# Optimization experiments

Measured on AMD Instinct MI355X. Metric: run time of the kernel, lower is better.

The kernel has to match this reference:

```python
import jax, jax.numpy as jnp
import numpy as np

EPS = 1e-5
K = 3  # involution kernel size


def bin_act(x):
    # STE binary activation: forward = sign(x), backward via piecewise poly
    m1 = (x < -1).astype(jnp.float32)
    m2 = (x < 0).astype(jnp.float32)
    m3 = (x < 1).astype(jnp.float32)
    out = -1.0 * m1 + (x * x + 2 * x) * (1 - m1)
    out = out * m2 + (-x * x + 2 * x) * (1 - m2)
    out = out * m3 + 1.0 * (1 - m3)
    sg = jax.lax.stop_gradient
    return sg(jnp.sign(x)) - sg(out) + out


def bin_conv1x1(x, w):
    # BinaryConv with kernel_size=1: w is (O, I, 1, 1)
    sf = jnp.mean(jnp.abs(w), axis=(1, 2, 3), keepdims=True)
    bw = sf * jnp.sign(w)
    rw = jnp.clip(w, -1.0, 1.0)
    sg = jax.lax.stop_gradient
    f = sg(bw) - sg(rw) + rw  # (O, I, 1, 1)
    return jnp.einsum('oi,bihw->bohw', f[:, :, 0, 0], x)


def batchnorm(x, gamma, beta):
    # training-mode BN over (N, H, W) per channel, biased variance
    m = jnp.mean(x, axis=(0, 2, 3), keepdims=True)
    v = jnp.mean((x - m) ** 2, axis=(0, 2, 3), keepdims=True)
    xn = (x - m) * jax.lax.rsqrt(v + EPS)
    return gamma.reshape(1, -1, 1, 1) * xn + beta.reshape(1, -1, 1, 1)


def prelu(x, a):
    return jnp.maximum(x, 0) + a.reshape(1, -1, 1, 1) * jnp.minimum(x, 0)


def setup_inputs() -> dict:
    key = jax.random.key(0)
    ks = jax.random.split(key, 8)
    B, C, H, W = 8, 64, 128, 128
    Cr = C // 2           # reduce_rate = 2
    KK = K * K            # group = 1
    inp = {
        'x': jax.random.normal(ks[0], (B, C, H, W), dtype=jnp.float32),
        'pre_bias_b': jnp.zeros((1, C, 1, 1), jnp.float32),
        'pre_conv_w': jax.random.uniform(ks[1], (C, C, 1, 1), jnp.float32) * 0.001,
        'pre_gamma': jnp.ones((C,), jnp.float32),
        'pre_beta': jnp.zeros((C,), jnp.float32),
        'pre_a': jnp.full((C,), 0.25, jnp.float32),
        'mid_bias_b': jnp.zeros((1, C, 1, 1), jnp.float32),
        'reduce_w': jax.random.uniform(ks[2], (Cr, C, 1, 1), jnp.float32) * 0.001,
        'span_w': jax.random.uniform(ks[3], (KK, Cr, 1, 1), jnp.float32) * 0.001,
        'mid_gamma': jnp.ones((C,), jnp.float32),
        'mid_beta': jnp.zeros((C,), jnp.float32),
        'mid_a': jnp.full((C,), 0.25, jnp.float32),
        'post_bias_b': jnp.zeros((1, C, 1, 1), jnp.float32),
        'post_conv_w': jax.random.uniform(ks[4], (C, C, 1, 1), jnp.float32) * 0.001,
        'post_gamma': jnp.ones((C,), jnp.float32),
        'post_beta': jnp.zeros((C,), jnp.float32),
    }
    return inp


def reference(x, pre_bias_b, pre_conv_w, pre_gamma, pre_beta, pre_a,
              mid_bias_b, reduce_w, span_w, mid_gamma, mid_beta, mid_a,
              post_bias_b, post_conv_w, post_gamma, post_beta):
    B, C, H, W = x.shape
    h = bin_act(x)
    h = h + pre_bias_b
    h = bin_conv1x1(h, pre_conv_w)
    h = batchnorm(h, pre_gamma, pre_beta)
    h = prelu(h, pre_a)
    h = h + mid_bias_b
    # kernel branch (AvgPool2d(1,1) is identity for stride=1)
    ker = bin_conv1x1(bin_conv1x1(h, reduce_w), span_w)  # (B, K*K, H, W)
    # unfold: 3x3 patches, pad=1, stride=1 -> (B, C, K*K, H, W)
    hp = jnp.pad(h, ((0, 0), (0, 0), (1, 1), (1, 1)))
    patches = jnp.stack(
        [hp[:, :, i:i + H, j:j + W] for i in range(K) for j in range(K)],
        axis=2)
    out = jnp.sum(patches * ker[:, None, :, :, :], axis=2)  # (B, C, H, W)
    out = batchnorm(out, mid_gamma, mid_beta)
    out = jax.nn.relu(out)
    out = prelu(out, mid_a)
    out = out + post_bias_b
    out = bin_conv1x1(out, post_conv_w)
    out = batchnorm(out, post_gamma, post_beta)
    return out + x  # downsample is Identity (stride=1)
```

## Files before the change

### kernel.cpp

```cpp
#include <hip/hip_runtime.h>

#define B_   8
#define HW   16384
#define CHW  (64*HW)
#define NPIX (8*16384)
#define EPS_ 1e-5f

typedef unsigned short u16;
typedef unsigned int   u32;
typedef unsigned long long u64;
typedef __attribute__((ext_vector_type(8))) short bf16x8;
typedef __attribute__((ext_vector_type(4))) float f32x4;

__device__ __forceinline__ float sgnf(float v){ return (float)((v>0.f)-(v<0.f)); }
__device__ __forceinline__ float bf2f(u16 h){ return __uint_as_float(((u32)h)<<16); }
__device__ __forceinline__ u16 f2bf(float f){
    u32 u = __float_as_uint(f);
    u += 0x7fffu + ((u>>16)&1u);
    return (u16)(u>>16);
}
__device__ __forceinline__ u32 pack2(float a, float b){
    return (u32)f2bf(a) | ((u32)f2bf(b)<<16);
}

__device__ __forceinline__ void bn1_consts(const u32* __restrict__ cnt,
                                           const float* __restrict__ AB,
                                           const float* __restrict__ g,
                                           const float* __restrict__ be,
                                           const float* __restrict__ pa,
                                           const float* __restrict__ mb,
                                           float* kA, float* kB,
                                           float* al, float* mbl, int tid){
    if (tid < 64){
        float A  = AB[tid], Bv = AB[64+tid];
        float sp = (float)cnt[tid], sq = (float)cnt[64+tid];
        float mpc = sp * (1.f/(float)NPIX);
        float e2  = sq * (1.f/(float)NPIX);
        float mean = fmaf(A, mpc, Bv);
        float var  = A*A*fmaxf(e2 - mpc*mpc, 0.f);
        float sc = g[tid] * rsqrtf(var + EPS_);
        float sh = be[tid] - mean*sc;
        kA[tid] = sc*A;
        kB[tid] = fmaf(sc, Bv, sh);
        al[tid] = pa[tid];
        mbl[tid]= mb[tid];
    }
}

__global__ __launch_bounds__(576) void prep(
                     const float* __restrict__ pre_w, const float* __restrict__ pre_bias,
                     const float* __restrict__ red_w, const float* __restrict__ span_w,
                     const float* __restrict__ post_w,
                     u32* __restrict__ wb, float* __restrict__ AB,
                     u16* __restrict__ wqbf, float* __restrict__ M,
                     u32* __restrict__ cnt){
    __shared__ float sr[32], ss[9];
    int t = threadIdx.x;
    if (t < 128) cnt[t] = 0u;
    if (t < 64){
        float s = 0.f;
        for (int i = 0; i < 64; i++) s += fabsf(pre_w[t*64+i]);
        float alpha = s * (1.f/64.f);
        u32 b0 = 0, b1 = 0;
        for (int i = 0; i < 32; i++){
            b0 |= (__float_as_uint(pre_w[t*64+i])    >> 31) << i;
            b1 |= (__float_as_uint(pre_w[t*64+32+i]) >> 31) << i;
        }
        float c0 = 0.f;
        for (int i = 0; i < 64; i++)
            c0 += alpha * sgnf(pre_w[t*64+i]) * pre_bias[i];
        wb[2*t]   = b0;
        wb[2*t+1] = b1;
        AB[t]     = -2.f * alpha;
        AB[64+t]  = 64.f * alpha + c0;
    }
    if (t >= 64 && t < 128){
        int o = t - 64;
        float s2 = 0.f;
        for (int i = 0; i < 64; i++) s2 += fabsf(post_w[o*64+i]);
        s2 *= (1.f/64.f);
        for (int i = 0; i < 64; i++) wqbf[o*64+i] = f2bf(s2 * sgnf(post_w[o*64+i]));
    }
    if (t >= 128 && t < 160){
        int r = t - 128;
        float s = 0.f;
        for (int i = 0; i < 64; i++) s += fabsf(red_w[r*64+i]);
        sr[r] = s * (1.f/64.f);
    }
    if (t >= 160 && t < 169){
        int j = t - 160;
        float s = 0.f;
        for (int r = 0; r < 32; r++) s += fabsf(span_w[j*32+r]);
        ss[j] = s * (1.f/32.f);
    }
    __syncthreads();
    if (t < 576){
        int i = t / 9, j = t - (t/9)*9;
        float m = 0.f;
        for (int r = 0; r < 32; r++)
            m += sgnf(span_w[j*32+r]) * sr[r] * sgnf(red_w[r*64+i]);
        M[i*9+j] = ss[j] * m;
    }
}

__global__ __launch_bounds__(256) void packb(const float* __restrict__ x,
                                             const u32* __restrict__ wb,
                                             u32* __restrict__ cnt,
                                             uint2* __restrict__ sb){
    __shared__ u32 blo[4][64], bhi[4][64];
    __shared__ uint2 sbl[256];
    __shared__ u32 ps[256], qs[256];
    int tid  = threadIdx.x;
    int w    = tid >> 6, lane = tid & 63;
    int p0   = blockIdx.x*256 + w*64;
    int b    = p0 >> 14;
    int pix  = p0 & (HW-1);
    const float* xb = x + (size_t)b*CHW + pix + lane;

    float v[64];
#pragma unroll
    for (int c = 0; c < 64; c++) v[c] = xb[(size_t)c*HW];

#pragma unroll
    for (int c = 0; c < 64; c++){
        u64 bal = __ballot((int)(__float_as_uint(v[c]) >> 31));
        if (lane == c){
            blo[w][c] = (u32)bal;
            bhi[w][c] = (u32)(bal >> 32);
        }
    }
    __syncthreads();

    u32 m0 = 0, m1 = 0;
    int sh = lane & 31;
    bool hi = lane >= 32;
#pragma unroll
    for (int c = 0; c < 32; c++){
        u32 sel = hi ? bhi[w][c] : blo[w][c];
        m0 |= ((sel >> sh) & 1u) << c;
    }
#pragma unroll
    for (int c = 0; c < 32; c++){
        u32 sel = hi ? bhi[w][32+c] : blo[w][32+c];
        m1 |= ((sel >> sh) & 1u) << c;
    }
    sb[p0 + lane] = make_uint2(m0, m1);
    sbl[tid]      = make_uint2(m0, m1);
    __syncthreads();

    int o  = tid & 63;
    int qd = tid >> 6;
    u32 w0 = wb[2*o], w1 = wb[2*o+1];
    u32 sp = 0, sq = 0;
#pragma unroll 8
    for (int k = 0; k < 64; k++){
        uint2 vv = sbl[qd*64 + k];
        u32 pc = (u32)(__popc(vv.x ^ w0) + __popc(vv.y ^ w1));
        sp += pc;
        sq += pc*pc;
    }
    ps[qd*64 + o] = sp;
    qs[qd*64 + o] = sq;
    __syncthreads();
    if (tid < 64){
        u32 S = ps[tid] + ps[64+tid] + ps[128+tid] + ps[192+tid];
        u32 Q = qs[tid] + qs[64+tid] + qs[128+tid] + qs[192+tid];
        atomicAdd(&cnt[tid],    S);
        atomicAdd(&cnt[64+tid], Q);
    }
}

__global__ __launch_bounds__(256) void kerk(const uint2* __restrict__ sb,
                                            const u32* __restrict__ cnt,
                                            const float* __restrict__ AB,
                                            const u32* __restrict__ wb,
                                            const float* __restrict__ pre_g,
                                            const float* __restrict__ pre_b,
                                            const float* __restrict__ pa,
                                            const float* __restrict__ mb,
                                            const float* __restrict__ M,
                                            u16* __restrict__ ker){
    __shared__ float kA[64], kB[64], al[64], mbl[64];
    __shared__ u32 wbl[128];
    int tid = threadIdx.x;
    bn1_consts(cnt, AB, pre_g, pre_b, pa, mb, kA, kB, al, mbl, tid);
    if (tid < 128) wbl[tid] = wb[tid];
    __syncthreads();

    int p   = blockIdx.x*256 + tid;
    int b   = p >> 14;
    int pix = p & (HW-1);
    uint2 mv = sb[p];

    float acc[9];
#pragma unroll
    for (int j = 0; j < 9; j++) acc[j] = 0.f;
    for (int i = 0; i < 64; i++){
        u32 pc = (u32)(__popc(mv.x ^ wbl[2*i]) + __popc(mv.y ^ wbl[2*i+1]));
        float w = fmaf(kA[i], (float)pc, kB[i]);
        float z = fmaxf(w, 0.f) + al[i]*fminf(w, 0.f) + mbl[i];
#pragma unroll
        for (int j = 0; j < 9; j++)
            acc[j] = fmaf(M[i*9+j], z, acc[j]);
    }
    u16* kb = ker + (size_t)b*9*HW + pix;
#pragma unroll
    for (int j = 0; j < 9; j++) kb[(size_t)j*HW] = f2bf(acc[j]);
}

__global__ __launch_bounds__(256) void gatherk(const uint2* __restrict__ sb,
                                               const u32* __restrict__ cnt,
                                               const float* __restrict__ AB,
                                               const u32* __restrict__ wb,
                                               const float* __restrict__ pre_g,
                                               const float* __restrict__ pre_b,
                                               const float* __restrict__ pa,
                                               const float* __restrict__ mb,
                                               const u16* __restrict__ ker,
                                               u16* __restrict__ y2,
                                               float2* __restrict__ part2){
    __shared__ float kA[64], kB[64], al[64], mbl[64];
    __shared__ u32 wbl[128];
    __shared__ uint2 sbT[768];
    __shared__ float zr[8*6*132];
    __shared__ float2 rowsum[32];

    int tid = threadIdx.x;
    bn1_consts(cnt, AB, pre_g, pre_b, pa, mb, kA, kB, al, mbl, tid);
    if (tid < 128) wbl[tid] = wb[tid];
    if (tid < 96){
        int cc = tid / 12, rem = tid - cc*12, rr = rem >> 1, ed = rem & 1;
        zr[(cc*6 + rr)*132 + ed*129] = 0.f;
    }

    int bid = blockIdx.x;
    int b  = bid >> 8;
    int cg = (bid >> 5) & 7;
    int rg = bid & 31;
    int y0 = rg*4;
    int c0 = cg*8;

    const uint2* sbb = sb + (size_t)b*HW;
#pragma unroll
    for (int k = 0; k < 3; k++){
        int e  = tid + 256*k;
        int rr = e >> 7;
        int xx = e & 127;
        int gy = y0 + rr - 1;
        int gc = min(max(gy, 0), 127);
        sbT[e] = sbb[gc*128 + xx];
    }
    __syncthreads();

#pragma unroll
    for (int k = 0; k < 24; k++){
        int e  = tid + 256*k;
        int cc = e / 768;
        int r2 = e - cc*768;
        int rr = r2 >> 7;
        int xx = r2 & 127;
        int c  = c0 + cc;
        int gy = y0 + rr - 1;
        float z = 0.f;
        if ((unsigned)gy < 128u){
            uint2 v = sbT[rr*128 + xx];
            u32 pc = (u32)(__popc(v.x ^ wbl[2*c]) + __popc(v.y ^ wbl[2*c+1]));
            float w = fmaf(kA[c], (float)pc, kB[c]);
            z = fmaxf(w, 0.f) + al[c]*fminf(w, 0.f) + mbl[c];
        }
        zr[(cc*6 + rr)*132 + xx + 1] = z;
    }
    __syncthreads();

    {
        int lane2 = tid & 63;
        int wv    = tid >> 6;
        int x0    = lane2*2;
        int gp    = (y0 + wv)*128 + x0;

        float k0[9], k1[9];
        const u16* kb = ker + (size_t)b*9*HW + gp;
#pragma unroll
        for (int j = 0; j < 9; j++){
            u32 u = *reinterpret_cast<const u32*>(kb + (size_t)j*HW);
            k0[j] = __uint_as_float(u << 16);
            k1[j] = __uint_as_float(u & 0xffff0000u);
        }

        u32* yo = reinterpret_cast<u32*>(y2 + (size_t)(b*64 + c0)*HW + gp);
#pragma unroll
        for (int cc = 0; cc < 8; cc++){
            const float* zrow = &zr[(cc*6 + wv)*132 + x0];
            float o0 = 0.f, o1 = 0.f;
#pragma unroll
            for (int dy = 0; dy < 3; dy++){
                float2 za = *reinterpret_cast<const float2*>(zrow + dy*132);
                float2 zb = *reinterpret_cast<const float2*>(zrow + dy*132 + 2);
                o0 = fmaf(za.x, k0[dy*3+0], o0);
                o0 = fmaf(za.y, k0[dy*3+1], o0);
                o0 = fmaf(zb.x, k0[dy*3+2], o0);
                o1 = fmaf(za.y, k1[dy*3+0], o1);
                o1 = fmaf(zb.x, k1[dy*3+1], o1);
                o1 = fmaf(zb.y, k1[dy*3+2], o1);
            }
            yo[(size_t)cc*(HW/2)] = pack2(o0, o1);
            float sm = o0 + o1, qm = o0*o0 + o1*o1;
#pragma unroll
            for (int m = 1; m < 64; m <<= 1){
                sm += __shfl_xor(sm, m);
                qm += __shfl_xor(qm, m);
            }
            if (lane2 == 0) rowsum[wv*8 + cc] = make_float2(sm, qm);
        }
    }
    __syncthreads();
    if (tid < 8){
        float S = 0.f, Q = 0.f;
#pragma unroll
        for (int w = 0; w < 4; w++){
            float2 v = rowsum[w*8 + tid];
            S += v.x; Q += v.y;
        }
        part2[(size_t)(c0 + tid)*256 + (b*32 + rg)] = make_float2(S, Q);
    }
}

__global__ __launch_bounds__(256) void combinek(const float2* __restrict__ part,
                                                const float* __restrict__ gamma,
                                                const float* __restrict__ beta,
                                                float* __restrict__ scsh,
                                                int nsl){
    int c = blockIdx.x, tid = threadIdx.x;
    float S = 0.f, Q = 0.f;
    for (int k = tid; k < nsl; k += 256){
        float2 v = part[(size_t)c*nsl + k];
        S += v.x; Q += v.y;
    }
    for (int off = 32; off > 0; off >>= 1){
        S += __shfl_down(S, off);
        Q += __shfl_down(Q, off);
    }
    __shared__ float2 wp[4];
    if ((tid & 63) == 0) wp[tid>>6] = make_float2(S, Q);
    __syncthreads();
    if (tid == 0){
        float S2 = 0.f, Q2 = 0.f;
#pragma unroll
        for (int w = 0; w < 4; w++){ S2 += wp[w].x; Q2 += wp[w].y; }
        float mean = S2 * (1.f/(float)NPIX);
        float var  = fmaxf(Q2 * (1.f/(float)NPIX) - mean*mean, 0.f);
        float sc = gamma[c] * rsqrtf(var + EPS_);
        scsh[c]    = sc;
        scsh[64+c] = beta[c] - mean*sc;
    }
}

__global__ __launch_bounds__(256) void conv_post(const u16* __restrict__ y2,
                                                 const float* __restrict__ scsh_in,
                                                 const float* __restrict__ pbias,
                                                 const u16* __restrict__ wqbf,
                                                 u16* __restrict__ y3,
                                                 float2* __restrict__ part3){
    __shared__ u16 sB[256*64];
    __shared__ float scl[64], shl[64], pbl[64];

    int tid = threadIdx.x;
    if (tid < 64){
        scl[tid] = scsh_in[tid];
        shl[tid] = scsh_in[64+tid];
        pbl[tid] = pbias[tid];
    }
    __syncthreads();

    int b    = blockIdx.x >> 6;
    int pix0 = (blockIdx.x & 63) << 8;

    {
        int cp = tid & 31;
        int g  = tid >> 5;
        const u16* r0 = y2 + (size_t)(b*64 + 2*cp)*HW + pix0;
        const u16* r1 = r0 + HW;
        float s0 = scl[2*cp],   h0 = shl[2*cp],   p0 = pbl[2*cp];
        float s1 = scl[2*cp+1], h1 = shl[2*cp+1], p1 = pbl[2*cp+1];
#pragma unroll
        for (int it = 0; it < 4; it++){
            int oct = g + it*8;
            uint4 va = *reinterpret_cast<const uint4*>(r0 + oct*8);
            uint4 vb = *reinterpret_cast<const uint4*>(r1 + oct*8);
            u32 wa[4] = {va.x, va.y, va.z, va.w};
            u32 wc[4] = {vb.x, vb.y, vb.z, vb.w};
#pragma unroll
            for (int k = 0; k < 4; k++){
                int px = oct*8 + 2*k;
                float a0 = fmaf(s0, bf2f((u16)(wa[k] & 0xffffu)), h0);
                float a1 = fmaf(s0, bf2f((u16)(wa[k] >> 16)),     h0);
                float c0v= fmaf(s1, bf2f((u16)(wc[k] & 0xffffu)), h1);
                float c1v= fmaf(s1, bf2f((u16)(wc[k] >> 16)),     h1);
                a0 = fmaxf(a0, 0.f) + p0;  a1 = fmaxf(a1, 0.f) + p0;
                c0v= fmaxf(c0v,0.f) + p1;  c1v= fmaxf(c1v,0.f) + p1;
                int e0 = px*64     + ((2*cp) ^ ((px & 7) << 3));
                int e1 = (px+1)*64 + ((2*cp) ^ (((px+1) & 7) << 3));
                *reinterpret_cast<u32*>(&sB[e0]) = pack2(a0, c0v);
                *reinterpret_cast<u32*>(&sB[e1]) = pack2(a1, c1v);
            }
        }
    }

    int w  = tid >> 6;
    int l  = tid & 63;
    int lr = l & 15;
    int lk = l >> 4;

    bf16x8 af[4][2];
#pragma unroll
    for (int os = 0; os < 4; os++){
        int o = os*16 + lr;
#pragma unroll
        for (int kf = 0; kf < 2; kf++)
            af[os][kf] = *reinterpret_cast<const bf16x8*>(wqbf + o*64 + lk*8 + kf*32);
    }
    __syncthreads();

    f32x4 acc[4][4];
#pragma unroll
    for (int os = 0; os < 4; os++)
#pragma unroll
        for (int ns = 0; ns < 4; ns++)
            acc[os][ns] = (f32x4){0.f, 0.f, 0.f, 0.f};

#pragma unroll
    for (int ns = 0; ns < 4; ns++){
        int px  = w*64 + ns*16 + lr;
        int swz = (px & 7) << 3;
        bf16x8 b0 = *reinterpret_cast<const bf16x8*>(&sB[px*64 + ((lk*8)      ^ swz)]);
        bf16x8 b1 = *reinterpret_cast<const bf16x8*>(&sB[px*64 + ((lk*8 + 32) ^ swz)]);
#pragma unroll
        for (int os = 0; os < 4; os++){
            acc[os][ns] = __builtin_amdgcn_mfma_f32_16x16x32_bf16(af[os][0], b0, acc[os][ns], 0, 0, 0);
            acc[os][ns] = __builtin_amdgcn_mfma_f32_16x16x32_bf16(af[os][1], b1, acc[os][ns], 0, 0, 0);
        }
    }

    u16* yb = y3 + (size_t)(b*64)*HW + pix0;
#pragma unroll
    for (int os = 0; os < 4; os++){
#pragma unroll
        for (int ns = 0; ns < 4; ns++){
            int px = w*64 + ns*16 + lr;
#pragma unroll
            for (int r = 0; r < 4; r++){
                int o = os*16 + lk*4 + r;
                yb[(size_t)o*HW + px] = f2bf(acc[os][ns][r]);
            }
        }
    }

    __syncthreads();
    float2* wsum = (float2*)sB;
#pragma unroll
    for (int os = 0; os < 4; os++){
#pragma unroll
        for (int r = 0; r < 4; r++){
            float s = acc[os][0][r] + acc[os][1][r] + acc[os][2][r] + acc[os][3][r];
            float q = acc[os][0][r]*acc[os][0][r] + acc[os][1][r]*acc[os][1][r]
                    + acc[os][2][r]*acc[os][2][r] + acc[os][3][r]*acc[os][3][r];
#pragma unroll
            for (int m = 1; m < 16; m <<= 1){
                s += __shfl_xor(s, m);
                q += __shfl_xor(q, m);
            }
            if (lr == 0) wsum[w*64 + os*16 + lk*4 + r] = make_float2(s, q);
        }
    }
    __syncthreads();
    if (tid < 64){
        float S = 0.f, Q = 0.f;
#pragma unroll
        for (int ww = 0; ww < 4; ww++){
            float2 v = wsum[ww*64 + tid];
            S += v.x; Q += v.y;
        }
        part3[(size_t)tid*512 + blockIdx.x] = make_float2(S, Q);
    }
}

__global__ __launch_bounds__(256) void finalk(const u16* __restrict__ y3,
                                              const float* __restrict__ x,
                                              const float* __restrict__ scsh,
                                              float* __restrict__ out){
    __shared__ float scl[64], shl[64];
    int tid = threadIdx.x;
    if (tid < 64){ scl[tid] = scsh[tid]; shl[tid] = scsh[64+tid]; }
    __syncthreads();
#pragma unroll
    for (int it = 0; it < 4; it++){
        int i4 = blockIdx.x*1024 + it*256 + tid;
        int c  = (i4 >> 12) & 63;
        uint2  yv = reinterpret_cast<const uint2*>(y3)[i4];
        float4 bx = reinterpret_cast<const float4*>(x)[i4];
        float s = scl[c], t = shl[c];
        float4 r;
        r.x = fmaf(s, __uint_as_float(yv.x << 16),          t) + bx.x;
        r.y = fmaf(s, __uint_as_float(yv.x & 0xffff0000u),  t) + bx.y;
        r.z = fmaf(s, __uint_as_float(yv.y << 16),          t) + bx.z;
        r.w = fmaf(s, __uint_as_float(yv.y & 0xffff0000u),  t) + bx.w;
        reinterpret_cast<float4*>(out)[i4] = r;
    }
}

extern "C" void kernel_launch(void* const* d_in, const int* in_sizes, int n_in,
                              void* d_out, int out_size, void* d_ws, size_t ws_size,
                              hipStream_t stream){
    const float* x        = (const float*)d_in[0];
    const float* pre_bias = (const float*)d_in[1];
    const float* pre_w    = (const float*)d_in[2];
    const float* pre_g    = (const float*)d_in[3];
    const float* pre_b    = (const float*)d_in[4];
    const float* pre_a    = (const float*)d_in[5];
    const float* mid_bias = (const float*)d_in[6];
    const float* red_w    = (const float*)d_in[7];
    const float* span_w   = (const float*)d_in[8];
    const float* mid_g    = (const float*)d_in[9];
    const float* mid_b    = (const float*)d_in[10];
    const float* post_bias= (const float*)d_in[12];
    const float* post_w   = (const float*)d_in[13];
    const float* post_g   = (const float*)d_in[14];
    const float* post_b   = (const float*)d_in[15];

    float* ws    = (float*)d_ws;
    uint2* sb    = (uint2*)ws;
    u16*   y3b   = (u16*)(ws + 262144);
    u16*   kerb  = (u16*)(ws + 262144 + 4194304);
    u16*   wqbf  = (u16*)(ws + 5046272);
    float* M     = ws + 5048320;
    u32*   wb    = (u32*)(ws + 5048960);
    float* AB    = ws + 5049088;
    u32*   cnt   = (u32*)(ws + 5049216);
    float2* part2 = (float2*)(ws + 5049344);
    float2* part3 = part2 + 16384;
    float* scsh2 = ws + 5147648;
    float* scsh3 = ws + 5147776;

    u16*   y2b = (u16*)d_out;
    float* out = (float*)d_out;

    hipLaunchKernelGGL(prep, dim3(1), dim3(576), 0, stream,
                       pre_w, pre_bias, red_w, span_w, post_w, wb, AB, wqbf, M, cnt);
    hipLaunchKernelGGL(packb, dim3(NPIX/256), dim3(256), 0, stream,
                       x, wb, cnt, sb);
    hipLaunchKernelGGL(kerk, dim3(NPIX/256), dim3(256), 0, stream,
                       sb, cnt, AB, wb, pre_g, pre_b, pre_a, mid_bias, M, kerb);
    hipLaunchKernelGGL(gatherk, dim3(2048), dim3(256), 0, stream,
                       sb, cnt, AB, wb, pre_g, pre_b, pre_a, mid_bias, kerb,
                       y2b, part2);
    hipLaunchKernelGGL(combinek, dim3(64), dim3(256), 0, stream,
                       part2, mid_g, mid_b, scsh2, 256);
    hipLaunchKernelGGL(conv_post, dim3(512), dim3(256), 0, stream,
                       y2b, scsh2, post_bias, wqbf, y3b, part3);
    hipLaunchKernelGGL(combinek, dim3(64), dim3(256), 0, stream,
                       part3, post_g, post_b, scsh3, 512);
    hipLaunchKernelGGL(finalk, dim3(2048), dim3(256), 0, stream,
                       y3b, x, scsh3, out);
}
```

Before: 104.2 us.

## Fold weight prep and mid-BN combine into consumer kernels, drop prep launch

Removes the single-block prep kernel and the first combinek launch. Each consumer kernel now builds the binarized weights, scales and span/reduce matrix it needs in shared memory using wave reductions and ballots, and conv_post reduces part2 itself before its GEMM. This cuts two serialized launches and the slow single-block prep, which used one thread per row. The cost is redundant per-block weight preprocessing and extra syncs in every block, plus a memset replacing the counter zeroing.

```diff
diff --git a/kernel.cpp b/kernel.cpp
--- a/kernel.cpp
+++ b/kernel.cpp
@@ -23,8 +23,33 @@
     return (u32)f2bf(a) | ((u32)f2bf(b)<<16);
 }
 
+__device__ __forceinline__ void build_pre(const float* __restrict__ pre_w,
+                                          const float* __restrict__ pre_bias,
+                                          u32* wbl, float* ABl, int tid){
+    int w = tid >> 6, lane = tid & 63;
+#pragma unroll 4
+    for (int rr = 0; rr < 16; rr++){
+        int o = (w << 4) + rr;
+        float pw = pre_w[o*64 + lane];
+        float t = fabsf(pw);
+#pragma unroll
+        for (int m = 1; m < 64; m <<= 1) t += __shfl_xor(t, m);
+        float alpha = t * (1.f/64.f);
+        float ct = alpha * sgnf(pw) * pre_bias[lane];
+#pragma unroll
+        for (int m = 1; m < 64; m <<= 1) ct += __shfl_xor(ct, m);
+        u64 bal = __ballot((int)(__float_as_uint(pw) >> 31));
+        if (lane == 0){
+            wbl[2*o]   = (u32)bal;
+            wbl[2*o+1] = (u32)(bal >> 32);
+            ABl[o]     = -2.f * alpha;
+            ABl[64+o]  = 64.f * alpha + ct;
+        }
+    }
+}
+
 __device__ __forceinline__ void bn1_consts(const u32* __restrict__ cnt,
-                                           const float* __restrict__ AB,
+                                           const float* ABl,
                                            const float* __restrict__ g,
                                            const float* __restrict__ be,
                                            const float* __restrict__ pa,
@@ -32,7 +57,7 @@
                                            float* kA, float* kB,
                                            float* al, float* mbl, int tid){
     if (tid < 64){
-        float A  = AB[tid], Bv = AB[64+tid];
+        float A  = ABl[tid], Bv = ABl[64+tid];
         float sp = (float)cnt[tid], sq = (float)cnt[64+tid];
         float mpc = sp * (1.f/(float)NPIX);
         float e2  = sq * (1.f/(float)NPIX);
@@ -47,72 +72,26 @@
     }
 }
 
-__global__ __launch_bounds__(576) void prep(
-                     const float* __restrict__ pre_w, const float* __restrict__ pre_bias,
-                     const float* __restrict__ red_w, const float* __restrict__ span_w,
-                     const float* __restrict__ post_w,
-                     u32* __restrict__ wb, float* __restrict__ AB,
-                     u16* __restrict__ wqbf, float* __restrict__ M,
-                     u32* __restrict__ cnt){
-    __shared__ float sr[32], ss[9];
-    int t = threadIdx.x;
-    if (t < 128) cnt[t] = 0u;
-    if (t < 64){
-        float s = 0.f;
-        for (int i = 0; i < 64; i++) s += fabsf(pre_w[t*64+i]);
-        float alpha = s * (1.f/64.f);
-        u32 b0 = 0, b1 = 0;
-        for (int i = 0; i < 32; i++){
-            b0 |= (__float_as_uint(pre_w[t*64+i])    >> 31) << i;
-            b1 |= (__float_as_uint(pre_w[t*64+32+i]) >> 31) << i;
-        }
-        float c0 = 0.f;
-        for (int i = 0; i < 64; i++)
-            c0 += alpha * sgnf(pre_w[t*64+i]) * pre_bias[i];
-        wb[2*t]   = b0;
-        wb[2*t+1] = b1;
-        AB[t]     = -2.f * alpha;
-        AB[64+t]  = 64.f * alpha + c0;
-    }
-    if (t >= 64 && t < 128){
-        int o = t - 64;
-        float s2 = 0.f;
-        for (int i = 0; i < 64; i++) s2 += fabsf(post_w[o*64+i]);
-        s2 *= (1.f/64.f);
-        for (int i = 0; i < 64; i++) wqbf[o*64+i] = f2bf(s2 * sgnf(post_w[o*64+i]));
-    }
-    if (t >= 128 && t < 160){
-        int r = t - 128;
-        float s = 0.f;
-        for (int i = 0; i < 64; i++) s += fabsf(red_w[r*64+i]);
-        sr[r] = s * (1.f/64.f);
-    }
-    if (t >= 160 && t < 169){
-        int j = t - 160;
-        float s = 0.f;
-        for (int r = 0; r < 32; r++) s += fabsf(span_w[j*32+r]);
-        ss[j] = s * (1.f/32.f);
-    }
-    __syncthreads();
-    if (t < 576){
-        int i = t / 9, j = t - (t/9)*9;
-        float m = 0.f;
-        for (int r = 0; r < 32; r++)
-            m += sgnf(span_w[j*32+r]) * sr[r] * sgnf(red_w[r*64+i]);
-        M[i*9+j] = ss[j] * m;
-    }
-}
-
 __global__ __launch_bounds__(256) void packb(const float* __restrict__ x,
-                                             const u32* __restrict__ wb,
+                                             const float* __restrict__ pre_w,
                                              u32* __restrict__ cnt,
                                              uint2* __restrict__ sb){
+    __shared__ u32 wbl[128];
     __shared__ u32 blo[4][64], bhi[4][64];
     __shared__ uint2 sbl[256];
     __shared__ u32 ps[256], qs[256];
     int tid  = threadIdx.x;
     int w    = tid >> 6, lane = tid & 63;
-    int p0   = blockIdx.x*256 + w*64;
+
+#pragma unroll 4
+    for (int rr = 0; rr < 16; rr++){
+        int o = (w << 4) + rr;
+        float pw = pre_w[o*64 + lane];
+        u64 bal = __ballot((int)(__float_as_uint(pw) >> 31));
+        if (lane == 0){ wbl[2*o] = (u32)bal; wbl[2*o+1] = (u32)(bal >> 32); }
+    }
+
+    int p0   = blockIdx.x*256 + (w << 6);
     int b    = p0 >> 14;
     int pix  = p0 & (HW-1);
     const float* xb = x + (size_t)b*CHW + pix + lane;
@@ -150,7 +129,7 @@
 
     int o  = tid & 63;
     int qd = tid >> 6;
-    u32 w0 = wb[2*o], w1 = wb[2*o+1];
+    u32 w0 = wbl[2*o], w1 = wbl[2*o+1];
     u32 sp = 0, sq = 0;
 #pragma unroll 8
     for (int k = 0; k < 64; k++){
@@ -172,19 +151,63 @@
 
 __global__ __launch_bounds__(256) void kerk(const uint2* __restrict__ sb,
                                             const u32* __restrict__ cnt,
-                                            const float* __restrict__ AB,
-                                            const u32* __restrict__ wb,
+                                            const float* __restrict__ pre_w,
+                                            const float* __restrict__ pre_bias,
                                             const float* __restrict__ pre_g,
                                             const float* __restrict__ pre_b,
                                             const float* __restrict__ pa,
                                             const float* __restrict__ mb,
-                                            const float* __restrict__ M,
+                                            const float* __restrict__ red_w,
+                                            const float* __restrict__ span_w,
                                             u16* __restrict__ ker){
+    __shared__ u32 wbl[128];
+    __shared__ float ABl[128];
     __shared__ float kA[64], kB[64], al[64], mbl[64];
-    __shared__ u32 wbl[128];
-    int tid = threadIdx.x;
-    bn1_consts(cnt, AB, pre_g, pre_b, pa, mb, kA, kB, al, mbl, tid);
-    if (tid < 128) wbl[tid] = wb[tid];
+    __shared__ float srl[32], ssl[9], Ml[576];
+    __shared__ u32 rs[64], ssg[9];
+    int tid = threadIdx.x, w = tid >> 6, lane = tid & 63;
+
+    build_pre(pre_w, pre_bias, wbl, ABl, tid);
+#pragma unroll 2
+    for (int rr = 0; rr < 8; rr++){
+        int r = (w << 3) + rr;
+        float rw = red_w[r*64 + lane];
+        float t = fabsf(rw);
+#pragma unroll
+        for (int m = 1; m < 64; m <<= 1) t += __shfl_xor(t, m);
+        u64 bal = __ballot((int)(__float_as_uint(rw) >> 31));
+        if (lane == 0){
+            srl[r] = t * (1.f/64.f);
+            rs[2*r] = (u32)bal; rs[2*r+1] = (u32)(bal >> 32);
+        }
+    }
+    if (w < 3){
+        for (int jj = 0; jj < 3; jj++){
+            int j = w*3 + jj;
+            float sw = (lane < 32) ? span_w[j*32 + lane] : 0.f;
+            float t = fabsf(sw);
+#pragma unroll
+            for (int m = 1; m < 64; m <<= 1) t += __shfl_xor(t, m);
+            u64 bal = __ballot((int)(lane < 32 ? (__float_as_uint(sw) >> 31) : 0u));
+            if (lane == 0){ ssl[j] = t * (1.f/32.f); ssg[j] = (u32)bal; }
+        }
+    }
+    __syncthreads();
+
+    for (int e = tid; e < 576; e += 256){
+        int i = e / 9, j = e - i*9;
+        u32 sj = ssg[j];
+        float m = 0.f;
+#pragma unroll
+        for (int r = 0; r < 32; r++){
+            u32 br = (rs[2*r + (i >> 5)] >> (i & 31)) & 1u;
+            u32 bs = (sj >> r) & 1u;
+            float t = srl[r];
+            m += (bs ^ br) ? -t : t;
+        }
+        Ml[e] = ssl[j] * m;
+    }
+    bn1_consts(cnt, ABl, pre_g, pre_b, pa, mb, kA, kB, al, mbl, tid);
     __syncthreads();
 
     int p   = blockIdx.x*256 + tid;
@@ -197,11 +220,11 @@
     for (int j = 0; j < 9; j++) acc[j] = 0.f;
     for (int i = 0; i < 64; i++){
         u32 pc = (u32)(__popc(mv.x ^ wbl[2*i]) + __popc(mv.y ^ wbl[2*i+1]));
-        float w = fmaf(kA[i], (float)pc, kB[i]);
-        float z = fmaxf(w, 0.f) + al[i]*fminf(w, 0.f) + mbl[i];
+        float ww = fmaf(kA[i], (float)pc, kB[i]);
+        float z = fmaxf(ww, 0.f) + al[i]*fminf(ww, 0.f) + mbl[i];
 #pragma unroll
         for (int j = 0; j < 9; j++)
-            acc[j] = fmaf(M[i*9+j], z, acc[j]);
+            acc[j] = fmaf(Ml[i*9+j], z, acc[j]);
     }
     u16* kb = ker + (size_t)b*9*HW + pix;
 #pragma unroll
@@ -210,8 +233,8 @@
 
 __global__ __launch_bounds__(256) void gatherk(const uint2* __restrict__ sb,
                                                const u32* __restrict__ cnt,
-                                               const float* __restrict__ AB,
-                                               const u32* __restrict__ wb,
+                                               const float* __restrict__ pre_w,
+                                               const float* __restrict__ pre_bias,
                                                const float* __restrict__ pre_g,
                                                const float* __restrict__ pre_b,
                                                const float* __restrict__ pa,
@@ -219,19 +242,21 @@
                                                const u16* __restrict__ ker,
                                                u16* __restrict__ y2,
                                                float2* __restrict__ part2){
+    __shared__ u32 wbl[128];
+    __shared__ float ABl[128];
     __shared__ float kA[64], kB[64], al[64], mbl[64];
-    __shared__ u32 wbl[128];
     __shared__ uint2 sbT[768];
     __shared__ float zr[8*6*132];
     __shared__ float2 rowsum[32];
 
     int tid = threadIdx.x;
-    bn1_consts(cnt, AB, pre_g, pre_b, pa, mb, kA, kB, al, mbl, tid);
-    if (tid < 128) wbl[tid] = wb[tid];
+    build_pre(pre_w, pre_bias, wbl, ABl, tid);
     if (tid < 96){
         int cc = tid / 12, rem = tid - cc*12, rr = rem >> 1, ed = rem & 1;
         zr[(cc*6 + rr)*132 + ed*129] = 0.f;
     }
+    __syncthreads();
+    bn1_consts(cnt, ABl, pre_g, pre_b, pa, mb, kA, kB, al, mbl, tid);
 
     int bid = blockIdx.x;
     int b  = bid >> 8;
@@ -265,8 +290,8 @@
         if ((unsigned)gy < 128u){
             uint2 v = sbT[rr*128 + xx];
             u32 pc = (u32)(__popc(v.x ^ wbl[2*c]) + __popc(v.y ^ wbl[2*c+1]));
-            float w = fmaf(kA[c], (float)pc, kB[c]);
-            z = fmaxf(w, 0.f) + al[c]*fminf(w, 0.f) + mbl[c];
+            float ww = fmaf(kA[c], (float)pc, kB[c]);
+            z = fmaxf(ww, 0.f) + al[c]*fminf(ww, 0.f) + mbl[c];
         }
         zr[(cc*6 + rr)*132 + xx + 1] = z;
     }
@@ -325,50 +350,58 @@
     }
 }
 
-__global__ __launch_bounds__(256) void combinek(const float2* __restrict__ part,
-                                                const float* __restrict__ gamma,
-                                                const float* __restrict__ beta,
-                                                float* __restrict__ scsh,
-                                                int nsl){
-    int c = blockIdx.x, tid = threadIdx.x;
-    float S = 0.f, Q = 0.f;
-    for (int k = tid; k < nsl; k += 256){
-        float2 v = part[(size_t)c*nsl + k];
-        S += v.x; Q += v.y;
-    }
-    for (int off = 32; off > 0; off >>= 1){
-        S += __shfl_down(S, off);
-        Q += __shfl_down(Q, off);
-    }
-    __shared__ float2 wp[4];
-    if ((tid & 63) == 0) wp[tid>>6] = make_float2(S, Q);
-    __syncthreads();
-    if (tid == 0){
-        float S2 = 0.f, Q2 = 0.f;
-#pragma unroll
-        for (int w = 0; w < 4; w++){ S2 += wp[w].x; Q2 += wp[w].y; }
-        float mean = S2 * (1.f/(float)NPIX);
-        float var  = fmaxf(Q2 * (1.f/(float)NPIX) - mean*mean, 0.f);
-        float sc = gamma[c] * rsqrtf(var + EPS_);
-        scsh[c]    = sc;
-        scsh[64+c] = beta[c] - mean*sc;
-    }
-}
-
 __global__ __launch_bounds__(256) void conv_post(const u16* __restrict__ y2,
-                                                 const float* __restrict__ scsh_in,
+                                                 const float2* __restrict__ part2,
+                                                 const float* __restrict__ mid_g,
+                                                 const float* __restrict__ mid_b,
                                                  const float* __restrict__ pbias,
-                                                 const u16* __restrict__ wqbf,
+                                                 const float* __restrict__ post_w,
                                                  u16* __restrict__ y3,
                                                  float2* __restrict__ part3){
     __shared__ u16 sB[256*64];
+    __shared__ u16 sA[64*64];
     __shared__ float scl[64], shl[64], pbl[64];
 
-    int tid = threadIdx.x;
-    if (tid < 64){
-        scl[tid] = scsh_in[tid];
-        shl[tid] = scsh_in[64+tid];
-        pbl[tid] = pbias[tid];
+    int tid = threadIdx.x, w = tid >> 6, lane = tid & 63;
+
+#pragma unroll 4
+    for (int rr = 0; rr < 16; rr++){
+        int o = (w << 4) + rr;
+        float pw = post_w[o*64 + lane];
+        float t = fabsf(pw);
+#pragma unroll
+        for (int m = 1; m < 64; m <<= 1) t += __shfl_xor(t, m);
+        float bw = (t * (1.f/64.f)) * sgnf(pw);
+        int swz = (o & 7) << 3;
+        sA[o*64 + (lane ^ swz)] = f2bf(bw);
+    }
+
+    {
+        int c = tid & 63, q = tid >> 6;
+        float S = 0.f, Q = 0.f;
+        const float2* pc = part2 + (size_t)c*256 + q*64;
+#pragma unroll 8
+        for (int k = 0; k < 64; k++){
+            float2 v = pc[k];
+            S += v.x; Q += v.y;
+        }
+        float2* tmp = (float2*)sB;
+        tmp[q*64 + c] = make_float2(S, Q);
+        __syncthreads();
+        if (tid < 64){
+            float S2 = 0.f, Q2 = 0.f;
+#pragma unroll
+            for (int s = 0; s < 4; s++){
+                float2 v = tmp[s*64 + tid];
+                S2 += v.x; Q2 += v.y;
+            }
+            float mean = S2 * (1.f/(float)NPIX);
+            float var  = fmaxf(Q2 * (1.f/(float)NPIX) - mean*mean, 0.f);
+            float sc = mid_g[tid] * rsqrtf(var + EPS_);
+            scl[tid] = sc;
+            shl[tid] = mid_b[tid] - mean*sc;
+            pbl[tid] = pbias[tid];
+        }
     }
     __syncthreads();
 
@@ -406,7 +439,6 @@
         }
     }
 
-    int w  = tid >> 6;
     int l  = tid & 63;
     int lr = l & 15;
     int lk = l >> 4;
@@ -415,9 +447,10 @@
 #pragma unroll
     for (int os = 0; os < 4; os++){
         int o = os*16 + lr;
+        int swz = (o & 7) << 3;
 #pragma unroll
         for (int kf = 0; kf < 2; kf++)
-            af[os][kf] = *reinterpret_cast<const bf16x8*>(wqbf + o*64 + lk*8 + kf*32);
+            af[os][kf] = *reinterpret_cast<const bf16x8*>(&sA[o*64 + ((lk*8 + kf*32) ^ swz)]);
     }
     __syncthreads();
 
@@ -481,6 +514,36 @@
             S += v.x; Q += v.y;
         }
         part3[(size_t)tid*512 + blockIdx.x] = make_float2(S, Q);
+    }
+}
+
+__global__ __launch_bounds__(256) void combinek(const float2* __restrict__ part,
+                                                const float* __restrict__ gamma,
+                                                const float* __restrict__ beta,
+                                                float* __restrict__ scsh,
+                                                int nsl){
+    int c = blockIdx.x, tid = threadIdx.x;
+    float S = 0.f, Q = 0.f;
+    for (int k = tid; k < nsl; k += 256){
+        float2 v = part[(size_t)c*nsl + k];
+        S += v.x; Q += v.y;
+    }
+    for (int off = 32; off > 0; off >>= 1){
+        S += __shfl_down(S, off);
+        Q += __shfl_down(Q, off);
+    }
+    __shared__ float2 wp[4];
+    if ((tid & 63) == 0) wp[tid>>6] = make_float2(S, Q);
+    __syncthreads();
+    if (tid == 0){
+        float S2 = 0.f, Q2 = 0.f;
+#pragma unroll
+        for (int w = 0; w < 4; w++){ S2 += wp[w].x; Q2 += wp[w].y; }
+        float mean = S2 * (1.f/(float)NPIX);
+        float var  = fmaxf(Q2 * (1.f/(float)NPIX) - mean*mean, 0.f);
+        float sc = gamma[c] * rsqrtf(var + EPS_);
+        scsh[c]    = sc;
+        scsh[64+c] = beta[c] - mean*sc;
     }
 }
 
@@ -530,33 +593,26 @@
     float* ws    = (float*)d_ws;
     uint2* sb    = (uint2*)ws;
     u16*   y3b   = (u16*)(ws + 262144);
-    u16*   kerb  = (u16*)(ws + 262144 + 4194304);
-    u16*   wqbf  = (u16*)(ws + 5046272);
-    float* M     = ws + 5048320;
-    u32*   wb    = (u32*)(ws + 5048960);
-    float* AB    = ws + 5049088;
-    u32*   cnt   = (u32*)(ws + 5049216);
-    float2* part2 = (float2*)(ws + 5049344);
-    float2* part3 = part2 + 16384;
-    float* scsh2 = ws + 5147648;
-    float* scsh3 = ws + 5147776;
+    u16*   kerb  = (u16*)(ws + 4456448);
+    float2* part2 = (float2*)(ws + 5046272);
+    float2* part3 = (float2*)(ws + 5079040);
+    u32*   cnt   = (u32*)(ws + 5144576);
+    float* scsh3 = ws + 5144704;
 
     u16*   y2b = (u16*)d_out;
     float* out = (float*)d_out;
 
-    hipLaunchKernelGGL(prep, dim3(1), dim3(576), 0, stream,
-                       pre_w, pre_bias, red_w, span_w, post_w, wb, AB, wqbf, M, cnt);
+    hipMemsetAsync(cnt, 0, 512, stream);
     hipLaunchKernelGGL(packb, dim3(NPIX/256), dim3(256), 0, stream,
-                       x, wb, cnt, sb);
+                       x, pre_w, cnt, sb);
     hipLaunchKernelGGL(kerk, dim3(NPIX/256), dim3(256), 0, stream,
-                       sb, cnt, AB, wb, pre_g, pre_b, pre_a, mid_bias, M, kerb);
+                       sb, cnt, pre_w, pre_bias, pre_g, pre_b, pre_a, mid_bias,
+                       red_w, span_w, kerb);
     hipLaunchKernelGGL(gatherk, dim3(2048), dim3(256), 0, stream,
-                       sb, cnt, AB, wb, pre_g, pre_b, pre_a, mid_bias, kerb,
-                       y2b, part2);
-    hipLaunchKernelGGL(combinek, dim3(64), dim3(256), 0, stream,
-                       part2, mid_g, mid_b, scsh2, 256);
+                       sb, cnt, pre_w, pre_bias, pre_g, pre_b, pre_a, mid_bias,
+                       kerb, y2b, part2);
     hipLaunchKernelGGL(conv_post, dim3(512), dim3(256), 0, stream,
-                       y2b, scsh2, post_bias, wqbf, y3b, part3);
+                       y2b, part2, mid_g, mid_b, post_bias, post_w, y3b, part3);
     hipLaunchKernelGGL(combinek, dim3(64), dim3(256), 0, stream,
                        part3, post_g, post_b, scsh3, 512);
     hipLaunchKernelGGL(finalk, dim3(2048), dim3(256), 0, stream,
```

Result: slower. 141.9 us (+36.2%).

## Split packb channels across waves and spread BN counter atomics over banks

Applied to the files above, without the earlier changes.

The sign-packing kernel now gives each wave 16 channels of the same 64 pixels, where before each wave loaded all 64 channels for its own pixels. This replaces the ballot/transpose with per-thread bit packing through shared memory and uses four times as many blocks with fewer registers each. The popcount statistics are accumulated into 8 banked counter copies to reduce atomic contention, and the BN1 constant computation sums those banks. Workspace offsets move to make room for the larger counter array.

```diff
diff --git a/kernel.cpp b/kernel.cpp
--- a/kernel.cpp
+++ b/kernel.cpp
@@ -32,8 +32,14 @@
                                            float* kA, float* kB,
                                            float* al, float* mbl, int tid){
     if (tid < 64){
+        u32 spu = 0, squ = 0;
+#pragma unroll
+        for (int k = 0; k < 8; k++){
+            spu += cnt[k*128 + tid];
+            squ += cnt[k*128 + 64 + tid];
+        }
         float A  = AB[tid], Bv = AB[64+tid];
-        float sp = (float)cnt[tid], sq = (float)cnt[64+tid];
+        float sp = (float)spu, sq = (float)squ;
         float mpc = sp * (1.f/(float)NPIX);
         float e2  = sq * (1.f/(float)NPIX);
         float mean = fmaf(A, mpc, Bv);
@@ -56,7 +62,7 @@
                      u32* __restrict__ cnt){
     __shared__ float sr[32], ss[9];
     int t = threadIdx.x;
-    if (t < 128) cnt[t] = 0u;
+    for (int k = t; k < 1024; k += 576) cnt[k] = 0u;
     if (t < 64){
         float s = 0.f;
         for (int i = 0; i < 64; i++) s += fabsf(pre_w[t*64+i]);
@@ -107,54 +113,40 @@
                                              const u32* __restrict__ wb,
                                              u32* __restrict__ cnt,
                                              uint2* __restrict__ sb){
-    __shared__ u32 blo[4][64], bhi[4][64];
-    __shared__ uint2 sbl[256];
+    __shared__ u16 sgn[64*4];
+    __shared__ uint2 sbl[64];
     __shared__ u32 ps[256], qs[256];
     int tid  = threadIdx.x;
     int w    = tid >> 6, lane = tid & 63;
-    int p0   = blockIdx.x*256 + w*64;
+    int p0   = blockIdx.x * 64;
     int b    = p0 >> 14;
     int pix  = p0 & (HW-1);
-    const float* xb = x + (size_t)b*CHW + pix + lane;
-
-    float v[64];
-#pragma unroll
-    for (int c = 0; c < 64; c++) v[c] = xb[(size_t)c*HW];
-
-#pragma unroll
-    for (int c = 0; c < 64; c++){
-        u64 bal = __ballot((int)(__float_as_uint(v[c]) >> 31));
-        if (lane == c){
-            blo[w][c] = (u32)bal;
-            bhi[w][c] = (u32)(bal >> 32);
-        }
-    }
-    __syncthreads();
-
-    u32 m0 = 0, m1 = 0;
-    int sh = lane & 31;
-    bool hi = lane >= 32;
-#pragma unroll
-    for (int c = 0; c < 32; c++){
-        u32 sel = hi ? bhi[w][c] : blo[w][c];
-        m0 |= ((sel >> sh) & 1u) << c;
-    }
-#pragma unroll
-    for (int c = 0; c < 32; c++){
-        u32 sel = hi ? bhi[w][32+c] : blo[w][32+c];
-        m1 |= ((sel >> sh) & 1u) << c;
-    }
-    sb[p0 + lane] = make_uint2(m0, m1);
-    sbl[tid]      = make_uint2(m0, m1);
+
+    const float* xbase = x + (size_t)b*CHW + (size_t)(w*16)*HW + pix + lane;
+    float v[16];
+#pragma unroll
+    for (int k = 0; k < 16; k++) v[k] = xbase[(size_t)k*HW];
+    u32 bits = 0;
+#pragma unroll
+    for (int k = 0; k < 16; k++)
+        bits |= (__float_as_uint(v[k]) >> 31) << k;
+    sgn[lane*4 + w] = (u16)bits;
+    __syncthreads();
+
+    if (tid < 64){
+        uint2 q = *reinterpret_cast<const uint2*>(&sgn[tid*4]);
+        sb[p0 + tid] = q;
+        sbl[tid]     = q;
+    }
     __syncthreads();
 
     int o  = tid & 63;
     int qd = tid >> 6;
     u32 w0 = wb[2*o], w1 = wb[2*o+1];
     u32 sp = 0, sq = 0;
-#pragma unroll 8
-    for (int k = 0; k < 64; k++){
-        uint2 vv = sbl[qd*64 + k];
+#pragma unroll
+    for (int i = 0; i < 16; i++){
+        uint2 vv = sbl[qd*16 + i];
         u32 pc = (u32)(__popc(vv.x ^ w0) + __popc(vv.y ^ w1));
         sp += pc;
         sq += pc*pc;
@@ -165,8 +157,9 @@
     if (tid < 64){
         u32 S = ps[tid] + ps[64+tid] + ps[128+tid] + ps[192+tid];
         u32 Q = qs[tid] + qs[64+tid] + qs[128+tid] + qs[192+tid];
-        atomicAdd(&cnt[tid],    S);
-        atomicAdd(&cnt[64+tid], Q);
+        u32* bank = cnt + (blockIdx.x & 7)*128;
+        atomicAdd(&bank[tid],    S);
+        atomicAdd(&bank[64+tid], Q);
     }
 }
 
@@ -530,29 +523,29 @@
     float* ws    = (float*)d_ws;
     uint2* sb    = (uint2*)ws;
     u16*   y3b   = (u16*)(ws + 262144);
-    u16*   kerb  = (u16*)(ws + 262144 + 4194304);
+    u16*   kerb  = (u16*)(ws + 4456448);
     u16*   wqbf  = (u16*)(ws + 5046272);
     float* M     = ws + 5048320;
     u32*   wb    = (u32*)(ws + 5048960);
     float* AB    = ws + 5049088;
     u32*   cnt   = (u32*)(ws + 5049216);
-    float2* part2 = (float2*)(ws + 5049344);
-    float2* part3 = part2 + 16384;
-    float* scsh2 = ws + 5147648;
-    float* scsh3 = ws + 5147776;
+    float2* part2 = (float2*)(ws + 5050240);
+    float2* part3 = (float2*)(ws + 5083008);
+    float* scsh2 = ws + 5148544;
+    float* scsh3 = ws + 5148672;
 
     u16*   y2b = (u16*)d_out;
     float* out = (float*)d_out;
 
     hipLaunchKernelGGL(prep, dim3(1), dim3(576), 0, stream,
                        pre_w, pre_bias, red_w, span_w, post_w, wb, AB, wqbf, M, cnt);
-    hipLaunchKernelGGL(packb, dim3(NPIX/256), dim3(256), 0, stream,
+    hipLaunchKernelGGL(packb, dim3(NPIX/64), dim3(256), 0, stream,
                        x, wb, cnt, sb);
     hipLaunchKernelGGL(kerk, dim3(NPIX/256), dim3(256), 0, stream,
                        sb, cnt, AB, wb, pre_g, pre_b, pre_a, mid_bias, M, kerb);
     hipLaunchKernelGGL(gatherk, dim3(2048), dim3(256), 0, stream,
-                       sb, cnt, AB, wb, pre_g, pre_b, pre_a, mid_bias, kerb,
-                       y2b, part2);
+                       sb, cnt, AB, wb, pre_g, pre_b, pre_a, mid_bias,
+                       kerb, y2b, part2);
     hipLaunchKernelGGL(combinek, dim3(64), dim3(256), 0, stream,
                        part2, mid_g, mid_b, scsh2, 256);
     hipLaunchKernelGGL(conv_post, dim3(512), dim3(256), 0, stream,
@@ -560,5 +553,5 @@
     hipLaunchKernelGGL(combinek, dim3(64), dim3(256), 0, stream,
                        part3, post_g, post_b, scsh3, 512);
     hipLaunchKernelGGL(finalk, dim3(2048), dim3(256), 0, stream,
-                       y3b, x, scsh3, out);
-}
+                       y3b, x, part3 == nullptr ? scsh3 : scsh3, out);
+}
```

Measured after the change: 96.71 us. 7.2% less time.
